# Optimization experiments

Hardware: AMD Instinct MI355X
Metric: run time of the kernel (lower is better)

The kernel has to match this reference:

```python
import jax, jax.numpy as jnp
import numpy as np

B, T, C, H, D = 2048, 64, 64, 8, 64  # batch, block_size, n_embed, num_heads, head_size


def setup_inputs() -> dict:
    key = jax.random.key(0)
    ks = jax.random.split(key, 6)
    s = C ** -0.5  # approx torch Linear init scale
    x = jax.random.normal(ks[0], (B, T, C), dtype=jnp.float32)
    Wq = jax.random.uniform(ks[1], (H, C, D), jnp.float32, -s, s)  # per-head query weights (in, out)
    Wk = jax.random.uniform(ks[2], (H, C, D), jnp.float32, -s, s)
    Wv = jax.random.uniform(ks[3], (H, C, D), jnp.float32, -s, s)
    sp = (H * D) ** -0.5
    Wproj = jax.random.uniform(ks[4], (H * D, C), jnp.float32, -sp, sp)  # proj weight (in, out)
    bproj = jax.random.uniform(ks[5], (C,), jnp.float32, -sp, sp)
    return {"x": x, "Wq": Wq, "Wk": Wk, "Wv": Wv, "Wproj": Wproj, "bproj": bproj}


def reference(x, Wq, Wk, Wv, Wproj, bproj):
    # per-head projections, vectorized over heads (original loops over Head modules)
    q = jnp.einsum('btc,hcd->bhtd', x, Wq)
    k = jnp.einsum('btc,hcd->bhtd', x, Wk)
    v = jnp.einsum('btc,hcd->bhtd', x, Wv)
    scores = jnp.einsum('bhtd,bhsd->bhts', q, k) * (D ** -0.5)  # [B,H,T,T]
    causal = jnp.tril(jnp.ones((T, T), dtype=bool))
    scores = jnp.where(causal, scores, jnp.float32(-jnp.inf))
    wei = jax.nn.softmax(scores, axis=-1)  # dropout = identity in eval mode
    out = jnp.einsum('bhts,bhsd->bhtd', wei, v)
    out = out.transpose(0, 2, 1, 3).reshape(B, T, H * D)  # concat heads on last dim
    out = out @ Wproj + bproj  # output projection (dropout = identity in eval)
    return out
```

## Files before the change

### kernel.cpp

```cpp
#include <hip/hip_runtime.h>

typedef __bf16 bf16x8 __attribute__((ext_vector_type(8)));
typedef float f32x4 __attribute__((ext_vector_type(4)));
typedef unsigned short u16x4 __attribute__((ext_vector_type(4)));
typedef unsigned int u32x4 __attribute__((ext_vector_type(4)));

#define LDA 72

__device__ __forceinline__ unsigned short f2bf(float f) {
  __bf16 b = (__bf16)f;
  return __builtin_bit_cast(unsigned short, b);
}

__device__ __forceinline__ u16x4 pack4(f32x4 v) {
  u16x4 r;
  r[0] = f2bf(v[0]); r[1] = f2bf(v[1]); r[2] = f2bf(v[2]); r[3] = f2bf(v[3]);
  return r;
}

__device__ __forceinline__ bf16x8 frag8(const unsigned short* p) {
  typedef unsigned short u16x8v __attribute__((ext_vector_type(8)));
  return __builtin_bit_cast(bf16x8, *reinterpret_cast<const u16x8v*>(p));
}

#define MFMA(a, b, c) __builtin_amdgcn_mfma_f32_16x16x32_bf16(a, b, c, 0, 0, 0)

__device__ __forceinline__ void cfrag2bfrag(const f32x4 v[4], bf16x8 out[2]) {
  unsigned O[4][2];
  #pragma unroll
  for (int si = 0; si < 4; ++si) {
    u16x4 p = pack4(v[si]);
    O[si][0] = (unsigned)p[0] | ((unsigned)p[1] << 16);
    O[si][1] = (unsigned)p[2] | ((unsigned)p[3] << 16);
  }
  unsigned H[2][2][2];
  #pragma unroll
  for (int s1 = 0; s1 < 2; ++s1)
    #pragma unroll
    for (int d = 0; d < 2; ++d) {
      auto r = __builtin_amdgcn_permlane32_swap(O[2 * s1][d], O[2 * s1 + 1][d], false, false);
      H[s1][0][d] = r[0];
      H[s1][1][d] = r[1];
    }
  #pragma unroll
  for (int e1 = 0; e1 < 2; ++e1) {
    auto r0 = __builtin_amdgcn_permlane16_swap(H[e1][0][0], H[e1][1][0], false, false);
    auto r1 = __builtin_amdgcn_permlane16_swap(H[e1][0][1], H[e1][1][1], false, false);
    u32x4 f;
    f[0] = r0[0]; f[1] = r1[0]; f[2] = r0[1]; f[3] = r1[1];
    out[e1] = __builtin_bit_cast(bf16x8, f);
  }
}

__global__ __launch_bounds__(256) void fuse_pack(
    const float* __restrict__ Wq, const float* __restrict__ Wk,
    const float* __restrict__ Wv, const float* __restrict__ Wp,
    unsigned short* __restrict__ wf) {
  __shared__ float A[64 * 65];
  __shared__ float B[64 * 65];
  const int blk = blockIdx.x;
  const int t = blk >> 3, h = blk & 7;
  const int tid = threadIdx.x;
  const float* Asrc = (t ? Wv : Wq) + h * 4096;
  const float* Bsrc = (t ? Wp : Wk) + h * 4096;
  for (int i = tid; i < 4096; i += 256) {
    A[(i >> 6) * 65 + (i & 63)] = Asrc[i];
    B[(i >> 6) * 65 + (i & 63)] = Bsrc[i];
  }
  __syncthreads();
  unsigned short* dst = wf + blk * 4096;
  for (int o = 0; o < 16; ++o) {
    int idx = o * 256 + tid;
    int k = idx >> 6, n = idx & 63;
    float s = 0.f;
    if (t == 0) {
      for (int d = 0; d < 64; ++d) s += A[k * 65 + d] * B[n * 65 + d];
      s *= 0.18033688f;
    } else {
      for (int d = 0; d < 64; ++d) s += A[k * 65 + d] * B[d * 65 + n];
    }
    int kk = k >> 5, i = k & 7, lg = (k >> 3) & 3, si = n >> 4, l15 = n & 15;
    dst[((kk * 4 + si) * 64 + lg * 16 + l15) * 8 + i] = f2bf(s);
  }
}

__global__ __launch_bounds__(256, 2) void mha_fwd(
    const float* __restrict__ x, const unsigned short* __restrict__ wf,
    const float* __restrict__ bproj, float* __restrict__ out) {
  __shared__ __attribute__((aligned(16))) unsigned short Xs[4][64 * LDA];

  const int tid  = threadIdx.x;
  const int lane = tid & 63;
  const int w    = tid >> 6;
  const int l15  = lane & 15;
  const int g    = lane >> 4;
  const int kcol = 8 * g;

  const float* xb = x + (size_t)blockIdx.x * 16384;
  #pragma unroll
  for (int it = 0; it < 16; ++it) {
    int idx = it * 1024 + tid * 4;
    float4 v = *reinterpret_cast<const float4*>(xb + idx);
    f32x4 vv = {v.x, v.y, v.z, v.w};
    int bt = idx >> 12, rem = idx & 4095;
    *reinterpret_cast<u16x4*>(&Xs[bt][(rem >> 6) * LDA + (rem & 63)]) = pack4(vv);
  }
  __syncthreads();

  bf16x8 xf[2][4];
  #pragma unroll
  for (int cc = 0; cc < 2; ++cc)
    #pragma unroll
    for (int t = 0; t < 4; ++t)
      xf[cc][t] = frag8(&Xs[w][(t * 16 + l15) * LDA + cc * 32 + kcol]);

  f32x4 oacc[4][4];
  #pragma unroll
  for (int nt = 0; nt < 4; ++nt) {
    float bias = bproj[nt * 16 + l15];
    f32x4 bv = {bias, bias, bias, bias};
    #pragma unroll
    for (int mt = 0; mt < 4; ++mt) oacc[mt][nt] = bv;
  }

  for (int h = 0; h < 8; ++h) {
    const unsigned short* mf = wf + h * 4096;
    const unsigned short* nf = wf + 32768 + h * 4096;

    bf16x8 Mf[2][4], Nf[2][4];
    #pragma unroll
    for (int kk = 0; kk < 2; ++kk)
      #pragma unroll
      for (int ct = 0; ct < 4; ++ct) {
        Mf[kk][ct] = frag8(&mf[(kk * 4 + ct) * 512 + lane * 8]);
        Nf[kk][ct] = frag8(&nf[(kk * 4 + ct) * 512 + lane * 8]);
      }

    bf16x8 gB[2][4];
    #pragma unroll
    for (int mt = 0; mt < 4; ++mt) {
      f32x4 gc[4] = {};
      #pragma unroll
      for (int kk = 0; kk < 2; ++kk)
        #pragma unroll
        for (int ct = 0; ct < 4; ++ct)
          gc[ct] = MFMA(Mf[kk][ct], xf[kk][mt], gc[ct]);
      bf16x8 o2[2];
      cfrag2bfrag(gc, o2);
      gB[0][mt] = o2[0]; gB[1][mt] = o2[1];
    }

    bf16x8 pA[2][4];
    #pragma unroll
    for (int mt = 0; mt < 4; ++mt) {
      f32x4 sc[4] = {};
      #pragma unroll
      for (int cc = 0; cc < 2; ++cc)
        #pragma unroll
        for (int st = 0; st < 4; ++st)
          if (st <= mt)
            sc[st] = MFMA(xf[cc][st], gB[cc][mt], sc[st]);
      const int m = mt * 16 + l15;
      float sum = 0.f;
      #pragma unroll
      for (int st = 0; st < 4; ++st) {
        if (st < mt) {
          #pragma unroll
          for (int r = 0; r < 4; ++r) { float e = exp2f(sc[st][r]); sc[st][r] = e; sum += e; }
        } else if (st == mt) {
          #pragma unroll
          for (int r = 0; r < 4; ++r) {
            int s = st * 16 + 4 * g + r;
            float e = (s <= m) ? exp2f(sc[st][r]) : 0.f;
            sc[st][r] = e; sum += e;
          }
        }
      }
      sum += __shfl_xor(sum, 16);
      sum += __shfl_xor(sum, 32);
      float rinv = __builtin_amdgcn_rcpf(sum);
      #pragma unroll
      for (int st = 0; st < 4; ++st)
        if (st <= mt) sc[st] *= rinv;
      bf16x8 o2[2];
      cfrag2bfrag(sc, o2);
      pA[0][mt] = o2[0]; pA[1][mt] = o2[1];
    }

    bf16x8 zB[2][4];
    #pragma unroll
    for (int nt = 0; nt < 4; ++nt) {
      f32x4 zc[4] = {};
      #pragma unroll
      for (int st = 0; st < 4; ++st) {
        zc[st] = MFMA(xf[0][st], Nf[0][nt], zc[st]);
        zc[st] = MFMA(xf[1][st], Nf[1][nt], zc[st]);
      }
      bf16x8 o2[2];
      cfrag2bfrag(zc, o2);
      zB[0][nt] = o2[0]; zB[1][nt] = o2[1];
    }

    #pragma unroll
    for (int mt = 0; mt < 4; ++mt)
      #pragma unroll
      for (int nt = 0; nt < 4; ++nt) {
        oacc[mt][nt] = MFMA(pA[0][mt], zB[0][nt], oacc[mt][nt]);
        if (mt >= 2)
          oacc[mt][nt] = MFMA(pA[1][mt], zB[1][nt], oacc[mt][nt]);
      }
  }

  float* ob = out + ((size_t)blockIdx.x * 4 + w) * 4096;
  #pragma unroll
  for (int mt = 0; mt < 4; ++mt)
    #pragma unroll
    for (int r = 0; r < 4; ++r) {
      float* orow = ob + (mt * 16 + 4 * g + r) * 64;
      #pragma unroll
      for (int nt = 0; nt < 4; ++nt)
        orow[nt * 16 + l15] = oacc[mt][nt][r];
    }
}

extern "C" void kernel_launch(void* const* d_in, const int* in_sizes, int n_in,
                              void* d_out, int out_size, void* d_ws, size_t ws_size,
                              hipStream_t stream) {
  const float* x  = (const float*)d_in[0];
  const float* Wq = (const float*)d_in[1];
  const float* Wk = (const float*)d_in[2];
  const float* Wv = (const float*)d_in[3];
  const float* Wp = (const float*)d_in[4];
  const float* bp = (const float*)d_in[5];
  unsigned short* wf = (unsigned short*)d_ws;

  fuse_pack<<<dim3(16), dim3(256), 0, stream>>>(Wq, Wk, Wv, Wp, wf);
  mha_fwd<<<dim3(512), dim3(256), 0, stream>>>(x, wf, bp, (float*)d_out);
}
```

Baseline: 57.90 us.

## Split heads across wave pairs and reduce partial outputs through shared memory

New measurement: 125.5 us. 2.17x slower.

```diff
diff --git a/kernel.cpp b/kernel.cpp
--- a/kernel.cpp
+++ b/kernel.cpp
@@ -84,46 +84,52 @@
   }
 }
 
-__global__ __launch_bounds__(256, 2) void mha_fwd(
+__global__ __launch_bounds__(256, 4) void mha_fwd(
     const float* __restrict__ x, const unsigned short* __restrict__ wf,
     const float* __restrict__ bproj, float* __restrict__ out) {
-  __shared__ __attribute__((aligned(16))) unsigned short Xs[4][64 * LDA];
+  __shared__ __attribute__((aligned(16))) unsigned char smem[32768];
+  unsigned short* XsBase = reinterpret_cast<unsigned short*>(smem);
 
   const int tid  = threadIdx.x;
   const int lane = tid & 63;
   const int w    = tid >> 6;
+  const int bt   = w & 1;
+  const int hh   = w >> 1;
   const int l15  = lane & 15;
   const int g    = lane >> 4;
   const int kcol = 8 * g;
 
-  const float* xb = x + (size_t)blockIdx.x * 16384;
-  #pragma unroll
-  for (int it = 0; it < 16; ++it) {
+  const float* xb = x + (size_t)blockIdx.x * 8192;
+  #pragma unroll
+  for (int it = 0; it < 8; ++it) {
     int idx = it * 1024 + tid * 4;
     float4 v = *reinterpret_cast<const float4*>(xb + idx);
     f32x4 vv = {v.x, v.y, v.z, v.w};
-    int bt = idx >> 12, rem = idx & 4095;
-    *reinterpret_cast<u16x4*>(&Xs[bt][(rem >> 6) * LDA + (rem & 63)]) = pack4(vv);
-  }
-  __syncthreads();
-
+    int sb = idx >> 12, rem = idx & 4095;
+    *reinterpret_cast<u16x4*>(&XsBase[sb * (64 * LDA) + (rem >> 6) * LDA + (rem & 63)]) = pack4(vv);
+  }
+  __syncthreads();
+
+  const unsigned short* Xmy = XsBase + bt * (64 * LDA);
   bf16x8 xf[2][4];
   #pragma unroll
   for (int cc = 0; cc < 2; ++cc)
     #pragma unroll
     for (int t = 0; t < 4; ++t)
-      xf[cc][t] = frag8(&Xs[w][(t * 16 + l15) * LDA + cc * 32 + kcol]);
+      xf[cc][t] = frag8(&Xmy[(t * 16 + l15) * LDA + cc * 32 + kcol]);
+  __syncthreads();
 
   f32x4 oacc[4][4];
   #pragma unroll
   for (int nt = 0; nt < 4; ++nt) {
-    float bias = bproj[nt * 16 + l15];
+    float bias = hh ? 0.f : bproj[nt * 16 + l15];
     f32x4 bv = {bias, bias, bias, bias};
     #pragma unroll
     for (int mt = 0; mt < 4; ++mt) oacc[mt][nt] = bv;
   }
 
-  for (int h = 0; h < 8; ++h) {
+  const int h0 = hh * 4;
+  for (int h = h0; h < h0 + 4; ++h) {
     const unsigned short* mf = wf + h * 4096;
     const unsigned short* nf = wf + 32768 + h * 4096;
 
@@ -211,16 +217,29 @@
       }
   }
 
-  float* ob = out + ((size_t)blockIdx.x * 4 + w) * 4096;
-  #pragma unroll
-  for (int mt = 0; mt < 4; ++mt)
-    #pragma unroll
-    for (int r = 0; r < 4; ++r) {
-      float* orow = ob + (mt * 16 + 4 * g + r) * 64;
+  float* fbuf = reinterpret_cast<float*>(smem) + bt * 4096;
+  if (hh == 1) {
+    #pragma unroll
+    for (int mt = 0; mt < 4; ++mt)
       #pragma unroll
       for (int nt = 0; nt < 4; ++nt)
-        orow[nt * 16 + l15] = oacc[mt][nt][r];
-    }
+        *reinterpret_cast<f32x4*>(&fbuf[((mt * 4 + nt) * 64 + lane) * 4]) = oacc[mt][nt];
+  }
+  __syncthreads();
+  if (hh == 0) {
+    float* ob = out + ((size_t)blockIdx.x * 2 + bt) * 4096;
+    #pragma unroll
+    for (int mt = 0; mt < 4; ++mt)
+      #pragma unroll
+      for (int r = 0; r < 4; ++r) {
+        float* orow = ob + (mt * 16 + 4 * g + r) * 64;
+        #pragma unroll
+        for (int nt = 0; nt < 4; ++nt) {
+          f32x4 other = *reinterpret_cast<const f32x4*>(&fbuf[((mt * 4 + nt) * 64 + lane) * 4]);
+          orow[nt * 16 + l15] = oacc[mt][nt][r] + other[r];
+        }
+      }
+  }
 }
 
 extern "C" void kernel_launch(void* const* d_in, const int* in_sizes, int n_in,
@@ -235,5 +254,5 @@
   unsigned short* wf = (unsigned short*)d_ws;
 
   fuse_pack<<<dim3(16), dim3(256), 0, stream>>>(Wq, Wk, Wv, Wp, wf);
-  mha_fwd<<<dim3(512), dim3(256), 0, stream>>>(x, wf, bp, (float*)d_out);
-}
+  mha_fwd<<<dim3(1024), dim3(256), 0, stream>>>(x, wf, bp, (float*)d_out);
+}
```
